# Performance work log

Measured on AMD Instinct MI355X. Metric: run time of the kernel, lower is better.

Reference implementation:

```python
import jax, jax.numpy as jnp
import numpy as np

DIM = 2048
HID = 5632  # multiple_of*ceil((2/3*8192)/256)
CONV = 4
SEQ = 8192


def setup_inputs() -> dict:
    key = jax.random.key(0)
    ks = jax.random.split(key, 6)
    x = jax.random.normal(ks[0], (1, SEQ, DIM), dtype=jnp.float32)
    cu_seqlens = jnp.array([0, 2048, 4096, 6144, 8192], dtype=jnp.int32)
    s = DIM ** -0.5
    w_w = jax.random.normal(ks[1], (HID, DIM), dtype=jnp.float32) * s
    wz_w = jax.random.normal(ks[2], (HID, DIM), dtype=jnp.float32) * s
    wh_w = jax.random.normal(ks[3], (HID, DIM), dtype=jnp.float32) * s
    wo_w = jax.random.normal(ks[4], (DIM, HID), dtype=jnp.float32) * (HID ** -0.5)
    conv_w = jax.random.normal(ks[5], (HID, CONV), dtype=jnp.float32) * (CONV ** -0.5)
    return {"x": x, "cu_seqlens": cu_seqlens, "w_w": w_w, "wz_w": wz_w,
            "wh_w": wh_w, "wo_w": wo_w, "conv_w": conv_w}


def _segment_ids(cu_seqlens, seq_len):
    start = jnp.zeros((seq_len,), dtype=jnp.int32).at[cu_seqlens[:-1]].set(1)
    return start, jnp.cumsum(start)  # start marker, segment id per position


def _causal_conv(z, conv_w, seg_id):
    # z: (b, s, H); depthwise causal conv, w[:, -1] multiplies current step,
    # masked so taps never cross cu_seqlens boundaries.
    s = z.shape[1]
    out = z * conv_w[:, CONV - 1][None, None, :]
    for k in range(1, CONV):
        zs = jnp.pad(z, ((0, 0), (k, 0), (0, 0)))[:, :s]
        sid = jnp.pad(seg_id, (k, 0))[:s]
        valid = (sid == seg_id) & (jnp.arange(s) >= k)
        out = out + zs * conv_w[:, CONV - 1 - k][None, None, :] * valid[None, :, None].astype(z.dtype)
    return out


def _linear_scan(a, b):
    # h_t = a_t * h_{t-1} + b_t along axis=1, via parallel associative scan
    def combine(l, r):
        al, bl = l
        ar, br = r
        return ar * al, ar * bl + br
    _, h = jax.lax.associative_scan(combine, (a, b), axis=1)
    return h


def reference(x, cu_seqlens, w_w, wz_w, wh_w, wo_w, conv_w):
    bsz, seq_len, _ = x.shape
    w0 = jnp.einsum('bsd,hd->bsh', x, w_w)
    z = jnp.einsum('bsd,hd->bsh', x, wz_w)
    tilde_h = jnp.einsum('bsd,hd->bsh', x, wh_w)
    start, seg_id = _segment_ids(cu_seqlens, seq_len)
    z = jax.nn.sigmoid(_causal_conv(z, conv_w, seg_id))
    a = (1.0 - z) * (1 - start)[None, :, None].astype(z.dtype)  # reset state at seq starts
    b = z * tilde_h
    h = _linear_scan(a, b)
    h = h * jax.nn.silu(w0)
    return jnp.einsum('bsh,dh->bsd', h, wo_w)
```

## Files before the change

### kernel.cpp

```cpp
#include <hip/hip_runtime.h>
#include <stdint.h>

#define DIM 2048
#define HID 5632
#define SEQ 8192
#define NW3 (3*HID)
#define CONV 4
#define CHUNK 64

typedef __attribute__((ext_vector_type(8))) __bf16 bf16x8;
typedef __attribute__((ext_vector_type(4))) float f32x4;

__device__ __forceinline__ uint16_t f2bf(float f) {
  union { float f; uint32_t u; } v; v.f = f;
  return (uint16_t)((v.u + 0x7FFFu + ((v.u >> 16) & 1u)) >> 16);
}
__device__ __forceinline__ float bf2f(uint16_t h) {
  union { uint32_t u; float f; } v; v.u = ((uint32_t)h) << 16;
  return v.f;
}

__global__ void cvt4_kernel(const float* __restrict__ src, uint16_t* __restrict__ dst, int n4) {
  int i = blockIdx.x * blockDim.x + threadIdx.x;
  if (i >= n4) return;
  float4 v = ((const float4*)src)[i];
  ushort4 o;
  o.x = f2bf(v.x); o.y = f2bf(v.y); o.z = f2bf(v.z); o.w = f2bf(v.w);
  ((ushort4*)dst)[i] = o;
}

__device__ __forceinline__ void load_lds16(const void* g, void* l) {
  __builtin_amdgcn_global_load_lds(
      (__attribute__((address_space(1))) void*)g,
      (__attribute__((address_space(3))) void*)l, 16, 0, 0);
}

template<int LDA, int LDB, int LDC, int KLEN, int OUT_MODE>
__global__ __launch_bounds__(512, 2)
void gemm256(const uint16_t* __restrict__ A, const uint16_t* __restrict__ B,
             void* __restrict__ C, int nbx)
{
  __shared__ alignas(16) uint16_t As[2][2][256][32];
  __shared__ alignas(16) uint16_t Bs[2][2][256][32];
  constexpr int NT = KLEN / 64;

  const int tid  = threadIdx.x;
  const int wave = tid >> 6;
  const int lane = tid & 63;

  const int nwg = (int)gridDim.x;
  const int bid = (int)blockIdx.x;
  const int qq  = nwg >> 3, rr = nwg & 7;
  const int xcd = bid & 7, loc = bid >> 3;
  const int swz = (xcd < rr ? xcd*(qq+1) : rr*(qq+1) + (xcd-rr)*qq) + loc;
  const int row0 = (swz % nbx) * 256;
  const int col0 = (swz / nbx) * 256;

  const uint16_t* Ab = A + (size_t)blockIdx.y * KLEN;
  const uint16_t* Bb = B + (size_t)blockIdx.y * KLEN;

  const int wr = wave >> 2;
  const int wc = wave & 3;
  const int rm = lane & 15;
  const int kq8 = ((lane >> 4) ^ ((rm >> 1) & 3)) * 8;
  const int ri = wr*128 + rm;
  const int ci = wc*64 + rm;

  size_t offA0, offA1, offB0, offB1;
  {
    const int g0 = tid,       r0_ = g0 >> 2, k0_ = (g0 & 3) ^ ((r0_ >> 1) & 3);
    const int g1 = 512 + tid, r1_ = g1 >> 2, k1_ = (g1 & 3) ^ ((r1_ >> 1) & 3);
    offA0 = (size_t)(row0 + r0_)*LDA + k0_*8;
    offA1 = (size_t)(row0 + r1_)*LDA + k1_*8;
    offB0 = (size_t)(col0 + r0_)*LDB + k0_*8;
    offB1 = (size_t)(col0 + r1_)*LDB + k1_*8;
  }

#define STAGE_A(kt,h,buf) do {                                              \
    const size_t ko_ = (size_t)(kt)*64 + (size_t)(h)*32;                    \
    load_lds16(Ab + offA0 + ko_, &As[(buf)][(h)][wave*16][0]);              \
    load_lds16(Ab + offA1 + ko_, &As[(buf)][(h)][128 + wave*16][0]);        \
  } while (0)
#define STAGE_B(kt,h,buf) do {                                              \
    const size_t ko_ = (size_t)(kt)*64 + (size_t)(h)*32;                    \
    load_lds16(Bb + offB0 + ko_, &Bs[(buf)][(h)][wave*16][0]);              \
    load_lds16(Bb + offB1 + ko_, &Bs[(buf)][(h)][128 + wave*16][0]);        \
  } while (0)

  f32x4 acc[8][4];
  #pragma unroll
  for (int i = 0; i < 8; ++i)
    #pragma unroll
    for (int j = 0; j < 4; ++j) acc[i][j] = (f32x4){0.f,0.f,0.f,0.f};

  STAGE_A(0,0,0); STAGE_B(0,0,0);
  STAGE_A(0,1,0); STAGE_B(0,1,0);
  {
    const int t1 = (NT > 1) ? 1 : 0;
    STAGE_A(t1,0,1); STAGE_B(t1,0,1);
  }
  asm volatile("s_waitcnt vmcnt(8)" ::: "memory");
  __builtin_amdgcn_s_barrier();

  #pragma unroll 1
  for (int t = 0; t < NT; ++t) {
    const int c   = t & 1;
    const int tn1 = (t+1 < NT) ? t+1 : NT-1;
    const int tn2 = (t+2 < NT) ? t+2 : NT-1;
    bf16x8 af[4], bfr[4];

    #pragma unroll
    for (int i = 0; i < 4; ++i) af[i]  = *(const bf16x8*)&As[c][0][ri + i*16][kq8];
    #pragma unroll
    for (int j = 0; j < 4; ++j) bfr[j] = *(const bf16x8*)&Bs[c][0][ci + j*16][kq8];
    STAGE_A(tn1, 1, c^1);
    __builtin_amdgcn_s_barrier();
    asm volatile("s_waitcnt lgkmcnt(0)" ::: "memory");
    __builtin_amdgcn_sched_barrier(0);
    __builtin_amdgcn_s_setprio(1);
    #pragma unroll
    for (int i = 0; i < 4; ++i)
      #pragma unroll
      for (int j = 0; j < 4; ++j)
        acc[i][j] = __builtin_amdgcn_mfma_f32_16x16x32_bf16(af[i], bfr[j], acc[i][j], 0, 0, 0);
    __builtin_amdgcn_s_setprio(0);
    __builtin_amdgcn_s_barrier();

    #pragma unroll
    for (int i = 0; i < 4; ++i) af[i] = *(const bf16x8*)&As[c][0][ri + (i+4)*16][kq8];
    STAGE_B(tn1, 1, c^1);
    __builtin_amdgcn_s_barrier();
    asm volatile("s_waitcnt lgkmcnt(0)" ::: "memory");
    __builtin_amdgcn_sched_barrier(0);
    __builtin_amdgcn_s_setprio(1);
    #pragma unroll
    for (int i = 0; i < 4; ++i)
      #pragma unroll
      for (int j = 0; j < 4; ++j)
        acc[i+4][j] = __builtin_amdgcn_mfma_f32_16x16x32_bf16(af[i], bfr[j], acc[i+4][j], 0, 0, 0);
    __builtin_amdgcn_s_setprio(0);
    asm volatile("s_waitcnt vmcnt(8)" ::: "memory");
    __builtin_amdgcn_s_barrier();

    #pragma unroll
    for (int i = 0; i < 4; ++i) af[i]  = *(const bf16x8*)&As[c][1][ri + i*16][kq8];
    #pragma unroll
    for (int j = 0; j < 4; ++j) bfr[j] = *(const bf16x8*)&Bs[c][1][ci + j*16][kq8];
    STAGE_A(tn2, 0, c);
    __builtin_amdgcn_s_barrier();
    asm volatile("s_waitcnt lgkmcnt(0)" ::: "memory");
    __builtin_amdgcn_sched_barrier(0);
    __builtin_amdgcn_s_setprio(1);
    #pragma unroll
    for (int i = 0; i < 4; ++i)
      #pragma unroll
      for (int j = 0; j < 4; ++j)
        acc[i][j] = __builtin_amdgcn_mfma_f32_16x16x32_bf16(af[i], bfr[j], acc[i][j], 0, 0, 0);
    __builtin_amdgcn_s_setprio(0);
    __builtin_amdgcn_s_barrier();

    #pragma unroll
    for (int i = 0; i < 4; ++i) af[i] = *(const bf16x8*)&As[c][1][ri + (i+4)*16][kq8];
    STAGE_B(tn2, 0, c);
    __builtin_amdgcn_s_barrier();
    asm volatile("s_waitcnt lgkmcnt(0)" ::: "memory");
    __builtin_amdgcn_sched_barrier(0);
    __builtin_amdgcn_s_setprio(1);
    #pragma unroll
    for (int i = 0; i < 4; ++i)
      #pragma unroll
      for (int j = 0; j < 4; ++j)
        acc[i+4][j] = __builtin_amdgcn_mfma_f32_16x16x32_bf16(af[i], bfr[j], acc[i+4][j], 0, 0, 0);
    __builtin_amdgcn_s_setprio(0);
    asm volatile("s_waitcnt vmcnt(8)" ::: "memory");
    __builtin_amdgcn_s_barrier();
  }
#undef STAGE_A
#undef STAGE_B

  const int cr = (lane >> 4) * 4;
  const int cc = lane & 15;
  #pragma unroll
  for (int i = 0; i < 8; ++i)
    #pragma unroll
    for (int j = 0; j < 4; ++j) {
      const int r_ = row0 + wr*128 + i*16 + cr;
      const int c_ = col0 + wc*64  + j*16 + cc;
      #pragma unroll
      for (int r = 0; r < 4; ++r) {
        const float v = acc[i][j][r];
        const size_t idx = (size_t)(r_ + r)*LDC + c_;
        if (OUT_MODE == 1)      ((uint16_t*)C)[idx] = f2bf(v);
        else if (OUT_MODE == 2) atomicAdd((float*)C + idx, v);
        else                    ((float*)C)[idx] = v;
      }
    }
}


__device__ __forceinline__ void seg_info(const int* cuv, int ns, int t, int& ss, bool& st) {
  ss = 0; st = false;
  for (int i=0;i<ns;i++) { int cv = cuv[i]; if (cv<=t && cv>ss) ss=cv; if (cv==t) st=true; }
}

__global__ void scan_chunk(const uint16_t* __restrict__ G, int qstart,
                           const uint16_t* __restrict__ zprev,
                           const float* __restrict__ convw,
                           const int* __restrict__ cu, int ncu,
                           float* __restrict__ Ach, float* __restrict__ Bch)
{
  int h = blockIdx.x * blockDim.x + threadIdx.x;
  int c = blockIdx.y;
  if (h >= HID) return;
  const uint16_t* Z  = G + HID;
  const uint16_t* TH = G + 2*HID;
  float w0c = convw[h*4+0], w1c = convw[h*4+1], w2c = convw[h*4+2], w3c = convw[h*4+3];
  int cuv[8];
  int ns = ncu - 1; if (ns > 8) ns = 8;
  for (int i=0;i<ns;i++) cuv[i] = cu[i];
  int r0 = c * CHUNK;
  int t0 = qstart + r0;
  float z1, z2, z3;
  if (c == 0) {
    z1 = (t0-1 >= 0) ? bf2f(zprev[2*HID + h]) : 0.f;
    z2 = (t0-2 >= 0) ? bf2f(zprev[1*HID + h]) : 0.f;
    z3 = (t0-3 >= 0) ? bf2f(zprev[0*HID + h]) : 0.f;
  } else {
    z1 = bf2f(Z[(size_t)(r0-1)*NW3 + h]);
    z2 = bf2f(Z[(size_t)(r0-2)*NW3 + h]);
    z3 = bf2f(Z[(size_t)(r0-3)*NW3 + h]);
  }
  float Aacc = 1.f, Bacc = 0.f;
  for (int r = r0; r < r0 + CHUNK; ++r) {
    int t = qstart + r;
    float z0 = bf2f(Z[(size_t)r*NW3 + h]);
    float th = bf2f(TH[(size_t)r*NW3 + h]);
    int ss; bool st;
    seg_info(cuv, ns, t, ss, st);
    float s = z0*w3c;
    if (t-1 >= ss) s += z1*w2c;
    if (t-2 >= ss) s += z2*w1c;
    if (t-3 >= ss) s += z3*w0c;
    float zc = 1.f/(1.f + __expf(-s));
    float a = st ? 0.f : (1.f - zc);
    float b = zc * th;
    Aacc *= a;
    Bacc = a*Bacc + b;
    z3 = z2; z2 = z1; z1 = z0;
  }
  Ach[(size_t)c*HID + h] = Aacc;
  Bch[(size_t)c*HID + h] = Bacc;
}

__global__ void scan_combine(float* __restrict__ Ach, const float* __restrict__ Bch,
                             float* __restrict__ Sc, int first, int nchunk)
{
  int h = blockIdx.x * blockDim.x + threadIdx.x;
  if (h >= HID) return;
  float s = first ? 0.f : Sc[h];
  for (int c = 0; c < nchunk; ++c) {
    size_t idx = (size_t)c*HID + h;
    float a = Ach[idx], b = Bch[idx];
    Ach[idx] = s;
    s = a*s + b;
  }
  Sc[h] = s;
}

__global__ void scan_final(uint16_t* __restrict__ G, int qstart,
                           const uint16_t* __restrict__ zprev,
                           const float* __restrict__ convw,
                           const int* __restrict__ cu, int ncu,
                           const float* __restrict__ Hin)
{
  int h = blockIdx.x * blockDim.x + threadIdx.x;
  int c = blockIdx.y;
  if (h >= HID) return;
  const uint16_t* W0 = G;
  const uint16_t* Z  = G + HID;
  uint16_t*       TH = G + 2*HID;
  float w0c = convw[h*4+0], w1c = convw[h*4+1], w2c = convw[h*4+2], w3c = convw[h*4+3];
  int cuv[8];
  int ns = ncu - 1; if (ns > 8) ns = 8;
  for (int i=0;i<ns;i++) cuv[i] = cu[i];
  int r0 = c * CHUNK;
  int t0 = qstart + r0;
  float z1, z2, z3;
  if (c == 0) {
    z1 = (t0-1 >= 0) ? bf2f(zprev[2*HID + h]) : 0.f;
    z2 = (t0-2 >= 0) ? bf2f(zprev[1*HID + h]) : 0.f;
    z3 = (t0-3 >= 0) ? bf2f(zprev[0*HID + h]) : 0.f;
  } else {
    z1 = bf2f(Z[(size_t)(r0-1)*NW3 + h]);
    z2 = bf2f(Z[(size_t)(r0-2)*NW3 + h]);
    z3 = bf2f(Z[(size_t)(r0-3)*NW3 + h]);
  }
  float state = Hin[(size_t)c*HID + h];
  for (int r = r0; r < r0 + CHUNK; ++r) {
    int t = qstart + r;
    float z0 = bf2f(Z[(size_t)r*NW3 + h]);
    float th = bf2f(TH[(size_t)r*NW3 + h]);
    int ss; bool st;
    seg_info(cuv, ns, t, ss, st);
    float s = z0*w3c;
    if (t-1 >= ss) s += z1*w2c;
    if (t-2 >= ss) s += z2*w1c;
    if (t-3 >= ss) s += z3*w0c;
    float zc = 1.f/(1.f + __expf(-s));
    float a = st ? 0.f : (1.f - zc);
    float b = zc * th;
    state = a*state + b;
    float w0v = bf2f(W0[(size_t)r*NW3 + h]);
    float silu = w0v / (1.f + __expf(-w0v));
    TH[(size_t)r*NW3 + h] = f2bf(state * silu);
    z3 = z2; z2 = z1; z1 = z0;
  }
}

__global__ void save_ztail(const uint16_t* __restrict__ G, uint16_t* __restrict__ zprev, int qrows) {
  int i = blockIdx.x * blockDim.x + threadIdx.x;
  if (i >= 3*HID) return;
  int j = i / HID;
  int h = i - j*HID;
  zprev[i] = G[(size_t)(qrows-3+j)*NW3 + HID + h];
}

extern "C" void kernel_launch(void* const* d_in, const int* in_sizes, int n_in,
                              void* d_out, int out_size, void* d_ws, size_t ws_size,
                              hipStream_t stream) {
  const float* x     = (const float*)d_in[0];
  const int*   cu    = (const int*)d_in[1];
  const float* w_w   = (const float*)d_in[2];
  const float* wz_w  = (const float*)d_in[3];
  const float* wh_w  = (const float*)d_in[4];
  const float* wo_w  = (const float*)d_in[5];
  const float* convw = (const float*)d_in[6];
  const int ncu = in_sizes[1];
  float* out = (float*)d_out;

  const size_t base = 92331008ull;
  int qrows = 2048;
  if (ws_size >= base + 8192ull*38592ull) qrows = 8192;
  else if (ws_size >= base + 4096ull*38592ull) qrows = 4096;
  const int nq = SEQ / qrows;
  const int nchunk = qrows / CHUNK;

  char* p = (char*)d_ws;
  uint16_t* w3b  = (uint16_t*)p; p += (size_t)NW3*DIM*2;
  uint16_t* wob  = (uint16_t*)p; p += (size_t)DIM*HID*2;
  float*    Sc   = (float*)p;    p += (size_t)HID*4;
  uint16_t* zprev= (uint16_t*)p; p += (size_t)3*HID*2;
  uint16_t* xseg = (uint16_t*)p; p += (size_t)qrows*DIM*2;
  uint16_t* G    = (uint16_t*)p; p += (size_t)qrows*NW3*2;
  float*    Ach  = (float*)p;    p += (size_t)nchunk*HID*4;
  float*    Bch  = (float*)p;    p += (size_t)nchunk*HID*4;

  {
    int n4 = HID*DIM/4;
    cvt4_kernel<<<(n4+255)/256, 256, 0, stream>>>(w_w,  w3b, n4);
    cvt4_kernel<<<(n4+255)/256, 256, 0, stream>>>(wz_w, w3b + (size_t)HID*DIM, n4);
    cvt4_kernel<<<(n4+255)/256, 256, 0, stream>>>(wh_w, w3b + (size_t)2*HID*DIM, n4);
    n4 = DIM*HID/4;
    cvt4_kernel<<<(n4+255)/256, 256, 0, stream>>>(wo_w, wob, n4);
  }

  if (qrows < 8192)
    hipMemsetAsync(out, 0, (size_t)out_size * sizeof(float), stream);

  for (int s = 0; s < nq; ++s) {
    const int qstart = s * qrows;

    int n4 = qrows*DIM/4;
    cvt4_kernel<<<(n4+255)/256, 256, 0, stream>>>(x + (size_t)qstart*DIM, xseg, n4);

    {
      const int nbx = qrows / 256;
      gemm256<DIM, DIM, NW3, DIM, 1><<<dim3(nbx * (NW3/256), 1), 512, 0, stream>>>(
          xseg, w3b, G, nbx);
    }

    scan_chunk  <<<dim3(HID/256, nchunk), 256, 0, stream>>>(G, qstart, zprev, convw, cu, ncu, Ach, Bch);
    scan_combine<<<HID/256, 256, 0, stream>>>(Ach, Bch, Sc, s == 0 ? 1 : 0, nchunk);
    scan_final  <<<dim3(HID/256, nchunk), 256, 0, stream>>>(G, qstart, zprev, convw, cu, ncu, Ach);

    if (s + 1 < nq)
      save_ztail<<<(3*HID+255)/256, 256, 0, stream>>>(G, zprev, qrows);

    if (qrows == 8192) {
      gemm256<NW3, HID, DIM, HID, 0><<<dim3(32*(DIM/256), 1), 512, 0, stream>>>(
          G + 2*HID, wob, out + (size_t)qstart*DIM, 32);
    } else if (qrows == 4096) {
      gemm256<NW3, HID, DIM, HID/2, 2><<<dim3(16*(DIM/256), 2), 512, 0, stream>>>(
          G + 2*HID, wob, out + (size_t)qstart*DIM, 16);
    } else {
      gemm256<NW3, HID, DIM, HID/4, 2><<<dim3(8*(DIM/256), 4), 512, 0, stream>>>(
          G + 2*HID, wob, out + (size_t)qstart*DIM, 8);
    }
  }
}
```

Baseline: 1.659 ms.

## Double-buffer GEMM fragment registers to overlap LDS reads with MFMA

```diff
diff --git a/kernel.cpp b/kernel.cpp
--- a/kernel.cpp
+++ b/kernel.cpp
@@ -86,12 +86,15 @@
     load_lds16(Bb + offB0 + ko_, &Bs[(buf)][(h)][wave*16][0]);              \
     load_lds16(Bb + offB1 + ko_, &Bs[(buf)][(h)][128 + wave*16][0]);        \
   } while (0)
+#define PIN() __builtin_amdgcn_sched_barrier(0)
 
   f32x4 acc[8][4];
   #pragma unroll
   for (int i = 0; i < 8; ++i)
     #pragma unroll
     for (int j = 0; j < 4; ++j) acc[i][j] = (f32x4){0.f,0.f,0.f,0.f};
+
+  bf16x8 a0[4], a1[4], b0[4], b1[4];
 
   STAGE_A(0,0,0); STAGE_B(0,0,0);
   STAGE_A(0,1,0); STAGE_B(0,1,0);
@@ -101,82 +104,87 @@
   }
   asm volatile("s_waitcnt vmcnt(8)" ::: "memory");
   __builtin_amdgcn_s_barrier();
+  PIN();
+  #pragma unroll
+  for (int i = 0; i < 4; ++i) a0[i] = *(const bf16x8*)&As[0][0][ri + i*16][kq8];
+  #pragma unroll
+  for (int j = 0; j < 4; ++j) b0[j] = *(const bf16x8*)&Bs[0][0][ci + j*16][kq8];
 
   #pragma unroll 1
   for (int t = 0; t < NT; ++t) {
     const int c   = t & 1;
     const int tn1 = (t+1 < NT) ? t+1 : NT-1;
     const int tn2 = (t+2 < NT) ? t+2 : NT-1;
-    bf16x8 af[4], bfr[4];
-
-    #pragma unroll
-    for (int i = 0; i < 4; ++i) af[i]  = *(const bf16x8*)&As[c][0][ri + i*16][kq8];
-    #pragma unroll
-    for (int j = 0; j < 4; ++j) bfr[j] = *(const bf16x8*)&Bs[c][0][ci + j*16][kq8];
+
+    #pragma unroll
+    for (int i = 0; i < 4; ++i) a1[i] = *(const bf16x8*)&As[c][0][ri + (i+4)*16][kq8];
     STAGE_A(tn1, 1, c^1);
-    __builtin_amdgcn_s_barrier();
-    asm volatile("s_waitcnt lgkmcnt(0)" ::: "memory");
-    __builtin_amdgcn_sched_barrier(0);
+    asm volatile("s_waitcnt lgkmcnt(4)" ::: "memory");
+    PIN();
     __builtin_amdgcn_s_setprio(1);
     #pragma unroll
     for (int i = 0; i < 4; ++i)
       #pragma unroll
       for (int j = 0; j < 4; ++j)
-        acc[i][j] = __builtin_amdgcn_mfma_f32_16x16x32_bf16(af[i], bfr[j], acc[i][j], 0, 0, 0);
+        acc[i][j] = __builtin_amdgcn_mfma_f32_16x16x32_bf16(a0[i], b0[j], acc[i][j], 0, 0, 0);
     __builtin_amdgcn_s_setprio(0);
+    asm volatile("s_waitcnt vmcnt(6)" ::: "memory");
     __builtin_amdgcn_s_barrier();
-
-    #pragma unroll
-    for (int i = 0; i < 4; ++i) af[i] = *(const bf16x8*)&As[c][0][ri + (i+4)*16][kq8];
+    PIN();
+
+    #pragma unroll
+    for (int i = 0; i < 4; ++i) a0[i] = *(const bf16x8*)&As[c][1][ri + i*16][kq8];
+    #pragma unroll
+    for (int j = 0; j < 4; ++j) b1[j] = *(const bf16x8*)&Bs[c][1][ci + j*16][kq8];
     STAGE_B(tn1, 1, c^1);
-    __builtin_amdgcn_s_barrier();
-    asm volatile("s_waitcnt lgkmcnt(0)" ::: "memory");
-    __builtin_amdgcn_sched_barrier(0);
+    asm volatile("s_waitcnt lgkmcnt(8)" ::: "memory");
+    PIN();
     __builtin_amdgcn_s_setprio(1);
     #pragma unroll
     for (int i = 0; i < 4; ++i)
       #pragma unroll
       for (int j = 0; j < 4; ++j)
-        acc[i+4][j] = __builtin_amdgcn_mfma_f32_16x16x32_bf16(af[i], bfr[j], acc[i+4][j], 0, 0, 0);
+        acc[i+4][j] = __builtin_amdgcn_mfma_f32_16x16x32_bf16(a1[i], b0[j], acc[i+4][j], 0, 0, 0);
     __builtin_amdgcn_s_setprio(0);
-    asm volatile("s_waitcnt vmcnt(8)" ::: "memory");
     __builtin_amdgcn_s_barrier();
-
-    #pragma unroll
-    for (int i = 0; i < 4; ++i) af[i]  = *(const bf16x8*)&As[c][1][ri + i*16][kq8];
-    #pragma unroll
-    for (int j = 0; j < 4; ++j) bfr[j] = *(const bf16x8*)&Bs[c][1][ci + j*16][kq8];
+    PIN();
+
+    #pragma unroll
+    for (int i = 0; i < 4; ++i) a1[i] = *(const bf16x8*)&As[c][1][ri + (i+4)*16][kq8];
     STAGE_A(tn2, 0, c);
-    __builtin_amdgcn_s_barrier();
-    asm volatile("s_waitcnt lgkmcnt(0)" ::: "memory");
-    __builtin_amdgcn_sched_barrier(0);
+    asm volatile("s_waitcnt lgkmcnt(4)" ::: "memory");
+    PIN();
     __builtin_amdgcn_s_setprio(1);
     #pragma unroll
     for (int i = 0; i < 4; ++i)
       #pragma unroll
       for (int j = 0; j < 4; ++j)
-        acc[i][j] = __builtin_amdgcn_mfma_f32_16x16x32_bf16(af[i], bfr[j], acc[i][j], 0, 0, 0);
+        acc[i][j] = __builtin_amdgcn_mfma_f32_16x16x32_bf16(a0[i], b1[j], acc[i][j], 0, 0, 0);
     __builtin_amdgcn_s_setprio(0);
+    asm volatile("s_waitcnt vmcnt(6)" ::: "memory");
     __builtin_amdgcn_s_barrier();
-
-    #pragma unroll
-    for (int i = 0; i < 4; ++i) af[i] = *(const bf16x8*)&As[c][1][ri + (i+4)*16][kq8];
+    PIN();
+
+    #pragma unroll
+    for (int i = 0; i < 4; ++i) a0[i] = *(const bf16x8*)&As[c^1][0][ri + i*16][kq8];
+    #pragma unroll
+    for (int j = 0; j < 4; ++j) b0[j] = *(const bf16x8*)&Bs[c^1][0][ci + j*16][kq8];
     STAGE_B(tn2, 0, c);
-    __builtin_amdgcn_s_barrier();
-    asm volatile("s_waitcnt lgkmcnt(0)" ::: "memory");
-    __builtin_amdgcn_sched_barrier(0);
+    asm volatile("s_waitcnt lgkmcnt(8)" ::: "memory");
+    PIN();
     __builtin_amdgcn_s_setprio(1);
     #pragma unroll
     for (int i = 0; i < 4; ++i)
       #pragma unroll
       for (int j = 0; j < 4; ++j)
-        acc[i+4][j] = __builtin_amdgcn_mfma_f32_16x16x32_bf16(af[i], bfr[j], acc[i+4][j], 0, 0, 0);
+        acc[i+4][j] = __builtin_amdgcn_mfma_f32_16x16x32_bf16(a1[i], b1[j], acc[i+4][j], 0, 0, 0);
     __builtin_amdgcn_s_setprio(0);
-    asm volatile("s_waitcnt vmcnt(8)" ::: "memory");
     __builtin_amdgcn_s_barrier();
+    PIN();
   }
 #undef STAGE_A
 #undef STAGE_B
+#undef PIN
 
   const int cr = (lane >> 4) * 4;
   const int cc = lane & 15;
```

Measured after the change: 1.729 ms. 1.04x slower.
